# Optimization experiments

Measured on AMD Instinct MI355X. Metric: run time of the kernel, lower is better.

Reference implementation:

```python
import jax, jax.numpy as jnp
import numpy as np

N, E, F_IN, HID, NCLS, K, D = 50000, 800000, 128, 64, 16, 3, 2
EPS = 1e-15


def gmm_conv(x, src, dst, edge_attr, g, mu, sigma, root, bias):
    # x: [N, Fin]; g: [Fin, K*M]; mu, sigma: [K, D]; root: [Fin, M]; bias: [M]
    M = g.shape[1] // K
    h = x @ g                                        # [N, K*M]
    hj = h[src].reshape(-1, K, M)                    # edge gather [E, K, M]
    diff = edge_attr[:, None, :] - mu[None, :, :]    # [E, K, D]
    gauss = jnp.exp((-0.5 * diff * diff / (EPS + sigma[None] ** 2)).sum(-1))  # [E, K]
    msg = (hj * gauss[:, :, None]).sum(axis=1)       # [E, M]
    agg = jax.ops.segment_sum(msg, dst, num_segments=N)                  # scatter-add
    deg = jax.ops.segment_sum(jnp.ones(msg.shape[0], x.dtype), dst, num_segments=N)
    agg = agg / jnp.maximum(deg, 1.0)[:, None]       # mean aggregation
    return agg + x @ root + bias


def setup_inputs() -> dict:
    key = jax.random.key(0)
    ks = jax.random.split(key, 13)
    x = jax.random.normal(ks[0], (N, F_IN), jnp.float32)
    edge_index = jax.random.randint(ks[1], (2, E), 0, N, dtype=jnp.int64)
    edge_attr = jax.random.uniform(ks[2], (E, D), jnp.float32)
    s1 = 1.0 / np.sqrt(F_IN)
    s2 = 1.0 / np.sqrt(HID)
    return {
        "x": x,
        "edge_index": edge_index,
        "edge_attr": edge_attr,
        "g1": jax.random.normal(ks[3], (F_IN, K * HID), jnp.float32) * s1,
        "mu1": jax.random.normal(ks[4], (K, D), jnp.float32),
        "sigma1": jnp.ones((K, D), jnp.float32),
        "root1": jax.random.normal(ks[5], (F_IN, HID), jnp.float32) * s1,
        "b1": jnp.zeros((HID,), jnp.float32),
        "g2": jax.random.normal(ks[6], (HID, K * NCLS), jnp.float32) * s2,
        "mu2": jax.random.normal(ks[7], (K, D), jnp.float32),
        "sigma2": jnp.ones((K, D), jnp.float32),
        "root2": jax.random.normal(ks[8], (HID, NCLS), jnp.float32) * s2,
        "b2": jnp.zeros((NCLS,), jnp.float32),
    }


def reference(x, edge_index, edge_attr, g1, mu1, sigma1, root1, b1, g2, mu2, sigma2, root2, b2):
    # eval mode: dropout is identity
    src, dst = edge_index[0], edge_index[1]
    h = gmm_conv(x, src, dst, edge_attr, g1, mu1, sigma1, root1, b1)
    h = jax.nn.elu(h)
    out = gmm_conv(h, src, dst, edge_attr, g2, mu2, sigma2, root2, b2)
    return jax.nn.log_softmax(out, axis=1)
```

## Files before the change

### kernel.cpp

```cpp
#include <hip/hip_runtime.h>
#include <hip/hip_fp16.h>

#define EPS 1e-15f
#define BKT_SHIFT 7
#define BKT_SIZE 128
#define NBKT_MAX 512

typedef _Float16 v8h __attribute__((ext_vector_type(8)));
typedef float v4f __attribute__((ext_vector_type(4)));
typedef float v2f __attribute__((ext_vector_type(2)));

#if __has_builtin(__builtin_amdgcn_cvt_pk_f32_fp8) && __has_builtin(__builtin_amdgcn_cvt_pk_fp8_f32)
#define FP8_HW 1
#else
#define FP8_HW 0
#endif

__device__ __forceinline__ unsigned char f32_to_fp8(float v) {
#if FP8_HW
    int r = __builtin_amdgcn_cvt_pk_fp8_f32(v, v, 0, false);
    return (unsigned char)(r & 0xFF);
#else
    __half h = __float2half(v);
    unsigned short u; __builtin_memcpy(&u, &h, 2);
    int s = (u >> 15) << 7;
    int a = (u & 0x7FFF) + 0x40;
    if (a < (9 << 10)) return (unsigned char)s;
    int t = (a >> 7) - 64;
    if (t > 126) t = 126;
    return (unsigned char)(s | t);
#endif
}

__device__ __forceinline__ float2 fp8x2_to_f32(unsigned short w) {
#if FP8_HW
    v2f r = __builtin_amdgcn_cvt_pk_f32_fp8((int)w, false);
    return make_float2(r.x, r.y);
#else
    int b0 = w & 0xFF, b1 = w >> 8;
    unsigned short h0 = (unsigned short)((((b0 & 0x7F) + 64) << 7) | ((b0 & 0x80) << 8));
    unsigned short h1 = (unsigned short)((((b1 & 0x7F) + 64) << 7) | ((b1 & 0x80) << 8));
    __half x0, x1;
    __builtin_memcpy(&x0, &h0, 2);
    __builtin_memcpy(&x1, &h1, 2);
    return make_float2(__half2float(x0), __half2float(x1));
#endif
}

__device__ __forceinline__ int load_idx(const int* __restrict__ ei, int is64, int pos) {
    return is64 ? ei[(size_t)2 * pos] : ei[pos];
}

__device__ __forceinline__ int h2_as_int(__half2 h) {
    int w; __builtin_memcpy(&w, &h, 4); return w;
}
__device__ __forceinline__ __half2 int_as_h2(int w) {
    __half2 h; __builtin_memcpy(&h, &w, 4); return h;
}

__global__ void detect_kernel(const int* __restrict__ ei, int* __restrict__ flag,
                              int* __restrict__ bcnt, int nbkt) {
    __shared__ int any_odd;
    if (threadIdx.x == 0) any_odd = 0;
    __syncthreads();
    for (int u = threadIdx.x; u < nbkt; u += 256) bcnt[u] = 0;
    if (ei[2 * threadIdx.x + 1] != 0) atomicOr(&any_odd, 1);
    __syncthreads();
    if (threadIdx.x == 0) *flag = any_odd ? 0 : 1;
}

__global__ __launch_bounds__(256) void bhist_kernel(
    const int* __restrict__ ei, const int* __restrict__ flag,
    int* __restrict__ bcnt, int E, int nbkt) {
    __shared__ int cnt[NBKT_MAX];
    int t = threadIdx.x;
    for (int u = t; u < nbkt; u += 256) cnt[u] = 0;
    __syncthreads();
    int is64 = *flag;
    int e0 = blockIdx.x * 4096;
#pragma unroll
    for (int i = 0; i < 16; ++i) {
        int e = e0 + i * 256 + t;
        if (e < E) atomicAdd(&cnt[load_idx(ei, is64, E + e) >> BKT_SHIFT], 1);
    }
    __syncthreads();
    for (int u = t; u < nbkt; u += 256)
        if (cnt[u]) atomicAdd(&bcnt[u], cnt[u]);
}

__global__ void bscan_kernel(const int* __restrict__ bcnt, int* __restrict__ bbase,
                             int* __restrict__ bcursor, int* __restrict__ rowptrN,
                             int nbkt, int E) {
    __shared__ int s[512];
    int t = threadIdx.x;
    int v = (t < nbkt) ? bcnt[t] : 0;
    s[t] = v;
    __syncthreads();
    for (int o = 1; o < 512; o <<= 1) {
        int u = (t >= o) ? s[t - o] : 0;
        __syncthreads();
        s[t] += u;
        __syncthreads();
    }
    if (t < nbkt) { int ex = s[t] - v; bbase[t] = ex; bcursor[t] = ex; }
    if (t == 0) { bbase[nbkt] = E; *rowptrN = E; }
}

__global__ __launch_bounds__(1024) void pass1_kernel(
    const int* __restrict__ ei, const int* __restrict__ flag,
    const float2* __restrict__ ea, int* __restrict__ bcursor,
    int4* __restrict__ staging, int E, int nbkt) {
    __shared__ int lcnt[NBKT_MAX];
    __shared__ int lcur[NBKT_MAX];
    int t = threadIdx.x;
    if (t < nbkt) lcnt[t] = 0;
    __syncthreads();
    int is64 = *flag;
    int e0 = blockIdx.x * 8192;
    int eend = min(e0 + 8192, E);

    for (int e = e0 + t; e < eend; e += 1024)
        atomicAdd(&lcnt[load_idx(ei, is64, E + e) >> BKT_SHIFT], 1);
    __syncthreads();

    if (t < nbkt) {
        int c = lcnt[t];
        lcur[t] = c ? atomicAdd(&bcursor[t], c) : 0;
    }
    __syncthreads();

    for (int e = e0 + t; e < eend; e += 1024) {
        int src = load_idx(ei, is64, e);
        int dst = load_idx(ei, is64, E + e);
        float2 a = ea[e];
        int pos = atomicAdd(&lcur[dst >> BKT_SHIFT], 1);
        staging[pos] = make_int4(src, dst,
                                 __float_as_int(a.x), __float_as_int(a.y));
    }
}

__global__ __launch_bounds__(256) void pass2_kernel(
    const int4* __restrict__ staging, const int* __restrict__ bbase,
    const float* __restrict__ mu1, const float* __restrict__ sg1,
    const float* __restrict__ mu2, const float* __restrict__ sg2,
    int4* __restrict__ rec, int* __restrict__ rowptr, int N) {
    __shared__ int lcnt[BKT_SIZE];
    __shared__ int ssc[BKT_SIZE];
    __shared__ int lcur[BKT_SIZE];
    int b = blockIdx.x;
    int node0 = b << BKT_SHIFT;
    int t = threadIdx.x;
    int beg = bbase[b], end = bbase[b + 1];

    if (t < BKT_SIZE) lcnt[t] = 0;
    __syncthreads();
    for (int j = beg + t; j < end; j += 256)
        atomicAdd(&lcnt[staging[j].y & (BKT_SIZE - 1)], 1);
    __syncthreads();
    int v = (t < BKT_SIZE) ? lcnt[t] : 0;
    if (t < BKT_SIZE) ssc[t] = v;
    __syncthreads();
    for (int o = 1; o < BKT_SIZE; o <<= 1) {
        int u = (t < BKT_SIZE && t >= o) ? ssc[t - o] : 0;
        __syncthreads();
        if (t < BKT_SIZE) ssc[t] += u;
        __syncthreads();
    }
    if (t < BKT_SIZE) {
        int excl = beg + ssc[t] - v;
        lcur[t] = excl;
        if (node0 + t < N) rowptr[node0 + t] = excl;
    }
    __syncthreads();

    float m1x[3], m1y[3], i1x[3], i1y[3], m2x[3], m2y[3], i2x[3], i2y[3];
#pragma unroll
    for (int k = 0; k < 3; ++k) {
        m1x[k] = mu1[2 * k]; m1y[k] = mu1[2 * k + 1];
        float s0 = sg1[2 * k], s1 = sg1[2 * k + 1];
        i1x[k] = -0.5f / (EPS + s0 * s0); i1y[k] = -0.5f / (EPS + s1 * s1);
        m2x[k] = mu2[2 * k]; m2y[k] = mu2[2 * k + 1];
        s0 = sg2[2 * k]; s1 = sg2[2 * k + 1];
        i2x[k] = -0.5f / (EPS + s0 * s0); i2y[k] = -0.5f / (EPS + s1 * s1);
    }

    for (int j = beg + t; j < end; j += 256) {
        int4 p = staging[j];
        float ax = __int_as_float(p.z), ay = __int_as_float(p.w);
        float g1v[3], g2v[3];
#pragma unroll
        for (int k = 0; k < 3; ++k) {
            float d0 = ax - m1x[k], d1 = ay - m1y[k];
            g1v[k] = __expf(d0 * d0 * i1x[k] + d1 * d1 * i1y[k]);
            d0 = ax - m2x[k]; d1 = ay - m2y[k];
            g2v[k] = __expf(d0 * d0 * i2x[k] + d1 * d1 * i2y[k]);
        }
        int pos = atomicAdd(&lcur[p.y & (BKT_SIZE - 1)], 1);
        int4 r;
        r.x = p.x;
        r.y = h2_as_int(__floats2half2_rn(g1v[0], g1v[1]));
        r.z = h2_as_int(__floats2half2_rn(g1v[2], g2v[0]));
        r.w = h2_as_int(__floats2half2_rn(g2v[1], g2v[2]));
        rec[pos] = r;
    }
}

__global__ void bprep_kernel(const float* __restrict__ g1, const float* __restrict__ r1,
                             __half* __restrict__ Bprep) {
    int gid = blockIdx.x * 256 + threadIdx.x;
    if (gid >= 32768) return;
    int fi = gid >> 9;
    int lane = (gid >> 3) & 63;
    int i = gid & 7;
    int ks = fi & 3, cb = fi >> 2;
    int k = ks * 32 + (lane >> 4) * 8 + i;
    int c = cb * 16 + (lane & 15);
    float v = (c < 192) ? g1[k * 192 + c] : r1[k * 64 + (c - 192)];
    Bprep[gid] = __float2half(v);
}

__global__ __launch_bounds__(256) void gemm1_mfma(
    const float* __restrict__ A, const __half* __restrict__ Bprep,
    unsigned char* __restrict__ hw1k, __half* __restrict__ hw1r, int M) {
    __shared__ char a_lds[64 * 256];
    int row0 = blockIdx.x * 64;
    int tid = threadIdx.x;
    int wid = tid >> 6, lane = tid & 63;

    const float4* xf4 = reinterpret_cast<const float4*>(A);
#pragma unroll
    for (int j = 0; j < 8; ++j) {
        int g = j * 256 + tid;
        int r = g >> 5, c = g & 31;
        int gr = row0 + r;
        float4 f = (gr < M) ? xf4[(size_t)gr * 32 + c]
                            : make_float4(0.f, 0.f, 0.f, 0.f);
        int2 v;
        v.x = h2_as_int(__floats2half2_rn(f.x, f.y));
        v.y = h2_as_int(__floats2half2_rn(f.z, f.w));
        int byte = r * 256 + c * 8;
        byte ^= (r & 7) << 4;
        *reinterpret_cast<int2*>(&a_lds[byte]) = v;
    }

    v8h bf[2][4];
#pragma unroll
    for (int cf = 0; cf < 2; ++cf)
#pragma unroll
        for (int ks = 0; ks < 4; ++ks) {
            int cb = blockIdx.y * 8 + wid * 2 + cf;
            int fi = cb * 4 + ks;
            bf[cf][ks] = *reinterpret_cast<const v8h*>(Bprep + (size_t)fi * 512 + lane * 8);
        }

    __syncthreads();

    v4f acc[4][2] = {};
#pragma unroll
    for (int ks = 0; ks < 4; ++ks) {
        v8h af[4];
#pragma unroll
        for (int rf = 0; rf < 4; ++rf) {
            int r = rf * 16 + (lane & 15);
            int byte = r * 256 + ks * 64 + (lane >> 4) * 16;
            byte ^= (r & 7) << 4;
            af[rf] = *reinterpret_cast<const v8h*>(&a_lds[byte]);
        }
#pragma unroll
        for (int rf = 0; rf < 4; ++rf)
#pragma unroll
            for (int cf = 0; cf < 2; ++cf)
                acc[rf][cf] = __builtin_amdgcn_mfma_f32_16x16x32_f16(
                    af[rf], bf[cf][ks], acc[rf][cf], 0, 0, 0);
    }

#pragma unroll
    for (int rf = 0; rf < 4; ++rf)
#pragma unroll
        for (int cf = 0; cf < 2; ++cf) {
            int gc = blockIdx.y * 128 + wid * 32 + cf * 16 + (lane & 15);
#pragma unroll
            for (int i = 0; i < 4; ++i) {
                int gr = row0 + rf * 16 + (lane >> 4) * 4 + i;
                if (gr < M) {
                    float val = acc[rf][cf][i];
                    if (gc < 192)
                        hw1k[(size_t)gr * 192 + gc] = f32_to_fp8(val);
                    else
                        hw1r[(size_t)gr * 64 + (gc - 192)] = __float2half(val);
                }
            }
        }
}

__global__ __launch_bounds__(256) void agg1_fused(
    const int4* __restrict__ rec, const int* __restrict__ rowptr,
    const unsigned char* __restrict__ hw1k, const __half* __restrict__ hw1r,
    const float* __restrict__ b1, const float* __restrict__ g2,
    const float* __restrict__ r2, __half* __restrict__ hw2h, int N) {
    __shared__ float Wlds[64][64];
    __shared__ float h2s[8][64];
    int t = threadIdx.x;

    for (int i = t; i < 4096; i += 256) {
        int k = i >> 6, c = i & 63;
        Wlds[k][c] = (c < 48) ? g2[k * 48 + c] : r2[k * 16 + (c - 48)];
    }

    int node = (blockIdx.x * 256 + t) >> 5;
    int nl = (t >> 5) & 7;
    int l = t & 31;
    bool active = node < N;

    float ax0 = 0.f, ay0 = 0.f, ax1 = 0.f, ay1 = 0.f;
    int beg = 0, end = 0;
    if (active) { beg = rowptr[node]; end = rowptr[node + 1]; }
    int j = beg;
    for (; j + 3 < end; j += 4) {
        int4 r0 = rec[j], r1 = rec[j + 1], r2v = rec[j + 2], r3 = rec[j + 3];
        const unsigned short* p0 = reinterpret_cast<const unsigned short*>(
            hw1k + (size_t)r0.x * 192);
        const unsigned short* p1 = reinterpret_cast<const unsigned short*>(
            hw1k + (size_t)r1.x * 192);
        const unsigned short* p2 = reinterpret_cast<const unsigned short*>(
            hw1k + (size_t)r2v.x * 192);
        const unsigned short* p3 = reinterpret_cast<const unsigned short*>(
            hw1k + (size_t)r3.x * 192);
        unsigned short w00 = p0[l], w01 = p0[32 + l], w02 = p0[64 + l];
        unsigned short w10 = p1[l], w11 = p1[32 + l], w12 = p1[64 + l];
        unsigned short w20 = p2[l], w21 = p2[32 + l], w22 = p2[64 + l];
        unsigned short w30 = p3[l], w31 = p3[32 + l], w32 = p3[64 + l];
        __half2 ha0 = int_as_h2(r0.y), hb0 = int_as_h2(r0.z);
        __half2 ha1 = int_as_h2(r1.y), hb1 = int_as_h2(r1.z);
        __half2 ha2 = int_as_h2(r2v.y), hb2 = int_as_h2(r2v.z);
        __half2 ha3 = int_as_h2(r3.y), hb3 = int_as_h2(r3.z);
        {
            float g0 = __low2float(ha0), g1 = __high2float(ha0), gg2 = __low2float(hb0);
            float2 a = fp8x2_to_f32(w00), b = fp8x2_to_f32(w01), c = fp8x2_to_f32(w02);
            ax0 += g0 * a.x + g1 * b.x + gg2 * c.x;
            ay0 += g0 * a.y + g1 * b.y + gg2 * c.y;
        }
        {
            float g0 = __low2float(ha1), g1 = __high2float(ha1), gg2 = __low2float(hb1);
            float2 a = fp8x2_to_f32(w10), b = fp8x2_to_f32(w11), c = fp8x2_to_f32(w12);
            ax1 += g0 * a.x + g1 * b.x + gg2 * c.x;
            ay1 += g0 * a.y + g1 * b.y + gg2 * c.y;
        }
        {
            float g0 = __low2float(ha2), g1 = __high2float(ha2), gg2 = __low2float(hb2);
            float2 a = fp8x2_to_f32(w20), b = fp8x2_to_f32(w21), c = fp8x2_to_f32(w22);
            ax0 += g0 * a.x + g1 * b.x + gg2 * c.x;
            ay0 += g0 * a.y + g1 * b.y + gg2 * c.y;
        }
        {
            float g0 = __low2float(ha3), g1 = __high2float(ha3), gg2 = __low2float(hb3);
            float2 a = fp8x2_to_f32(w30), b = fp8x2_to_f32(w31), c = fp8x2_to_f32(w32);
            ax1 += g0 * a.x + g1 * b.x + gg2 * c.x;
            ay1 += g0 * a.y + g1 * b.y + gg2 * c.y;
        }
    }
    for (; j < end; ++j) {
        int4 r0 = rec[j];
        __half2 ha0 = int_as_h2(r0.y), hb0 = int_as_h2(r0.z);
        float g0 = __low2float(ha0), g1 = __high2float(ha0), gg2 = __low2float(hb0);
        const unsigned short* p0 = reinterpret_cast<const unsigned short*>(
            hw1k + (size_t)r0.x * 192);
        float2 a = fp8x2_to_f32(p0[l]);
        float2 b = fp8x2_to_f32(p0[32 + l]);
        float2 c = fp8x2_to_f32(p0[64 + l]);
        ax0 += g0 * a.x + g1 * b.x + gg2 * c.x;
        ay0 += g0 * a.y + g1 * b.y + gg2 * c.y;
    }
    if (active) {
        float d = fmaxf((float)(end - beg), 1.0f);
        float2 root = __half22float2(
            reinterpret_cast<const __half2*>(hw1r + (size_t)node * 64)[l]);
        float2 bb = reinterpret_cast<const float2*>(b1)[l];
        float v0 = (ax0 + ax1) / d + root.x + bb.x;
        float v1 = (ay0 + ay1) / d + root.y + bb.y;
        h2s[nl][2 * l]     = v0 > 0.f ? v0 : expm1f(v0);
        h2s[nl][2 * l + 1] = v1 > 0.f ? v1 : expm1f(v1);
    }
    __syncthreads();

    if (active) {
        float acc0 = 0.f, acc1 = 0.f;
#pragma unroll 8
        for (int k = 0; k < 64; ++k) {
            float hv = h2s[nl][k];
            float2 w = *reinterpret_cast<const float2*>(&Wlds[k][2 * l]);
            acc0 += hv * w.x;
            acc1 += hv * w.y;
        }
        reinterpret_cast<__half2*>(hw2h)[(size_t)node * 32 + l] =
            __floats2half2_rn(acc0, acc1);
    }
}

__global__ __launch_bounds__(256) void agg2_kernel(
    const int4* __restrict__ rec, const int* __restrict__ rowptr,
    const __half* __restrict__ hw2h, const float* __restrict__ b2,
    float* __restrict__ out, int N) {
    int node = (blockIdx.x * 256 + threadIdx.x) >> 3;
    int l = threadIdx.x & 7;
    if (node >= N) return;
    int beg = rowptr[node], end = rowptr[node + 1];
    float ax = 0.f, ay = 0.f;
    for (int j = beg; j < end; ++j) {
        int4 r = rec[j];
        __half2 hb = int_as_h2(r.z), hc = int_as_h2(r.w);
        float g0 = __high2float(hb), g1 = __low2float(hc), g2 = __high2float(hc);
        const __half2* p = reinterpret_cast<const __half2*>(hw2h + (size_t)r.x * 64);
        float2 f0 = __half22float2(p[l]);
        float2 f1 = __half22float2(p[8 + l]);
        float2 f2 = __half22float2(p[16 + l]);
        ax += g0 * f0.x + g1 * f1.x + g2 * f2.x;
        ay += g0 * f0.y + g1 * f1.y + g2 * f2.y;
    }
    float d = fmaxf((float)(end - beg), 1.0f);
    float2 root = __half22float2(
        reinterpret_cast<const __half2*>(hw2h + (size_t)node * 64 + 48)[l]);
    float2 bb = reinterpret_cast<const float2*>(b2)[l];
    float v0 = ax / d + root.x + bb.x;
    float v1 = ay / d + root.y + bb.y;

    float mx = fmaxf(v0, v1);
#pragma unroll
    for (int off = 4; off >= 1; off >>= 1) mx = fmaxf(mx, __shfl_xor(mx, off, 8));
    float s = __expf(v0 - mx) + __expf(v1 - mx);
#pragma unroll
    for (int off = 4; off >= 1; off >>= 1) s += __shfl_xor(s, off, 8);
    float ls = __logf(s);
    float2 o = make_float2(v0 - mx - ls, v1 - mx - ls);
    reinterpret_cast<float2*>(out + (size_t)node * 16)[l] = o;
}

extern "C" void kernel_launch(void* const* d_in, const int* in_sizes, int n_in,
                              void* d_out, int out_size, void* d_ws, size_t ws_size,
                              hipStream_t stream) {
    const float* x   = (const float*)d_in[0];
    const int*   ei  = (const int*)d_in[1];
    const float* ea  = (const float*)d_in[2];
    const float* g1  = (const float*)d_in[3];
    const float* mu1 = (const float*)d_in[4];
    const float* sg1 = (const float*)d_in[5];
    const float* r1  = (const float*)d_in[6];
    const float* b1  = (const float*)d_in[7];
    const float* g2  = (const float*)d_in[8];
    const float* mu2 = (const float*)d_in[9];
    const float* sg2 = (const float*)d_in[10];
    const float* r2  = (const float*)d_in[11];
    const float* b2  = (const float*)d_in[12];

    const int N = in_sizes[0] / 128;
    const int E = in_sizes[2] / 2;
    const int nbkt = (N + BKT_SIZE - 1) >> BKT_SHIFT;

    unsigned char* hw1k = (unsigned char*)d_ws;
    __half* hw1r = (__half*)(hw1k + (size_t)N * 192);
    __half* hw2h = (__half*)(hw1r + (size_t)N * 64);
    int4*   rec  = (int4*)(hw2h + (size_t)N * 64);
    int4*   staging = rec + E;
    __half* Bprep = (__half*)(staging + E);
    int*    rowptr  = (int*)(Bprep + 32768);
    int*    bcnt    = rowptr + N + 1;
    int*    bbase   = bcnt + nbkt;
    int*    bcursor = bbase + nbkt + 1;
    int*    flag    = bcursor + nbkt;

    detect_kernel<<<1, 256, 0, stream>>>(ei, flag, bcnt, nbkt);
    bhist_kernel<<<(E + 4095) / 4096, 256, 0, stream>>>(ei, flag, bcnt, E, nbkt);
    bscan_kernel<<<1, 512, 0, stream>>>(bcnt, bbase, bcursor, rowptr + N, nbkt, E);

    pass1_kernel<<<(E + 8191) / 8192, 1024, 0, stream>>>(
        ei, flag, (const float2*)ea, bcursor, staging, E, nbkt);
    pass2_kernel<<<nbkt, 256, 0, stream>>>(
        staging, bbase, mu1, sg1, mu2, sg2, rec, rowptr, N);

    bprep_kernel<<<128, 256, 0, stream>>>(g1, r1, Bprep);
    gemm1_mfma<<<dim3((N + 63) / 64, 2), 256, 0, stream>>>(x, Bprep, hw1k, hw1r, N);

    agg1_fused<<<((size_t)N * 32 + 255) / 256, 256, 0, stream>>>(
        rec, rowptr, hw1k, hw1r, b1, g2, r2, hw2h, N);

    agg2_kernel<<<((size_t)N * 8 + 255) / 256, 256, 0, stream>>>(
        rec, rowptr, hw2h, b2, (float*)d_out, N);
}
```

Before: 133.1 us.

## Balance agg1 edge work across block via LDS atomics with packed dst-local index

Instead of one 32-lane group per destination node walking its own edge list, each block now takes the contiguous edge range of its 8 nodes and spreads the edges round-robin over the 8 groups, accumulating into shared memory with float atomics. The local destination index is packed into the top byte of the source id in the edge record, and agg2 masks it off. This evens out work when node degrees differ, at the cost of LDS atomic contention, the loss of the 4-way unrolled loads, and a source id limited to 24 bits. Atomic ordering also makes the summation order nondeterministic.

```diff
diff --git a/kernel.cpp b/kernel.cpp
--- a/kernel.cpp
+++ b/kernel.cpp
@@ -195,9 +195,10 @@
             d0 = ax - m2x[k]; d1 = ay - m2y[k];
             g2v[k] = __expf(d0 * d0 * i2x[k] + d1 * d1 * i2y[k]);
         }
-        int pos = atomicAdd(&lcur[p.y & (BKT_SIZE - 1)], 1);
+        int dl = p.y & (BKT_SIZE - 1);
+        int pos = atomicAdd(&lcur[dl], 1);
         int4 r;
-        r.x = p.x;
+        r.x = p.x | (dl << 24);
         r.y = h2_as_int(__floats2half2_rn(g1v[0], g1v[1]));
         r.z = h2_as_int(__floats2half2_rn(g1v[2], g2v[0]));
         r.w = h2_as_int(__floats2half2_rn(g2v[1], g2v[2]));
@@ -299,101 +300,69 @@
     const float* __restrict__ b1, const float* __restrict__ g2,
     const float* __restrict__ r2, __half* __restrict__ hw2h, int N) {
     __shared__ float Wlds[64][64];
-    __shared__ float h2s[8][64];
+    __shared__ float h2a[8][64];
+    __shared__ int rp[9];
     int t = threadIdx.x;
+    int node0 = blockIdx.x * 8;
 
     for (int i = t; i < 4096; i += 256) {
         int k = i >> 6, c = i & 63;
         Wlds[k][c] = (c < 48) ? g2[k * 48 + c] : r2[k * 16 + (c - 48)];
     }
-
-    int node = (blockIdx.x * 256 + t) >> 5;
-    int nl = (t >> 5) & 7;
-    int l = t & 31;
-    bool active = node < N;
-
-    float ax0 = 0.f, ay0 = 0.f, ax1 = 0.f, ay1 = 0.f;
-    int beg = 0, end = 0;
-    if (active) { beg = rowptr[node]; end = rowptr[node + 1]; }
-    int j = beg;
-    for (; j + 3 < end; j += 4) {
-        int4 r0 = rec[j], r1 = rec[j + 1], r2v = rec[j + 2], r3 = rec[j + 3];
-        const unsigned short* p0 = reinterpret_cast<const unsigned short*>(
-            hw1k + (size_t)r0.x * 192);
-        const unsigned short* p1 = reinterpret_cast<const unsigned short*>(
-            hw1k + (size_t)r1.x * 192);
-        const unsigned short* p2 = reinterpret_cast<const unsigned short*>(
-            hw1k + (size_t)r2v.x * 192);
-        const unsigned short* p3 = reinterpret_cast<const unsigned short*>(
-            hw1k + (size_t)r3.x * 192);
-        unsigned short w00 = p0[l], w01 = p0[32 + l], w02 = p0[64 + l];
-        unsigned short w10 = p1[l], w11 = p1[32 + l], w12 = p1[64 + l];
-        unsigned short w20 = p2[l], w21 = p2[32 + l], w22 = p2[64 + l];
-        unsigned short w30 = p3[l], w31 = p3[32 + l], w32 = p3[64 + l];
-        __half2 ha0 = int_as_h2(r0.y), hb0 = int_as_h2(r0.z);
-        __half2 ha1 = int_as_h2(r1.y), hb1 = int_as_h2(r1.z);
-        __half2 ha2 = int_as_h2(r2v.y), hb2 = int_as_h2(r2v.z);
-        __half2 ha3 = int_as_h2(r3.y), hb3 = int_as_h2(r3.z);
-        {
-            float g0 = __low2float(ha0), g1 = __high2float(ha0), gg2 = __low2float(hb0);
-            float2 a = fp8x2_to_f32(w00), b = fp8x2_to_f32(w01), c = fp8x2_to_f32(w02);
-            ax0 += g0 * a.x + g1 * b.x + gg2 * c.x;
-            ay0 += g0 * a.y + g1 * b.y + gg2 * c.y;
-        }
-        {
-            float g0 = __low2float(ha1), g1 = __high2float(ha1), gg2 = __low2float(hb1);
-            float2 a = fp8x2_to_f32(w10), b = fp8x2_to_f32(w11), c = fp8x2_to_f32(w12);
-            ax1 += g0 * a.x + g1 * b.x + gg2 * c.x;
-            ay1 += g0 * a.y + g1 * b.y + gg2 * c.y;
-        }
-        {
-            float g0 = __low2float(ha2), g1 = __high2float(ha2), gg2 = __low2float(hb2);
-            float2 a = fp8x2_to_f32(w20), b = fp8x2_to_f32(w21), c = fp8x2_to_f32(w22);
-            ax0 += g0 * a.x + g1 * b.x + gg2 * c.x;
-            ay0 += g0 * a.y + g1 * b.y + gg2 * c.y;
-        }
-        {
-            float g0 = __low2float(ha3), g1 = __high2float(ha3), gg2 = __low2float(hb3);
-            float2 a = fp8x2_to_f32(w30), b = fp8x2_to_f32(w31), c = fp8x2_to_f32(w32);
-            ax1 += g0 * a.x + g1 * b.x + gg2 * c.x;
-            ay1 += g0 * a.y + g1 * b.y + gg2 * c.y;
-        }
-    }
-    for (; j < end; ++j) {
-        int4 r0 = rec[j];
-        __half2 ha0 = int_as_h2(r0.y), hb0 = int_as_h2(r0.z);
-        float g0 = __low2float(ha0), g1 = __high2float(ha0), gg2 = __low2float(hb0);
-        const unsigned short* p0 = reinterpret_cast<const unsigned short*>(
-            hw1k + (size_t)r0.x * 192);
-        float2 a = fp8x2_to_f32(p0[l]);
-        float2 b = fp8x2_to_f32(p0[32 + l]);
-        float2 c = fp8x2_to_f32(p0[64 + l]);
-        ax0 += g0 * a.x + g1 * b.x + gg2 * c.x;
-        ay0 += g0 * a.y + g1 * b.y + gg2 * c.y;
-    }
-    if (active) {
-        float d = fmaxf((float)(end - beg), 1.0f);
-        float2 root = __half22float2(
-            reinterpret_cast<const __half2*>(hw1r + (size_t)node * 64)[l]);
-        float2 bb = reinterpret_cast<const float2*>(b1)[l];
-        float v0 = (ax0 + ax1) / d + root.x + bb.x;
-        float v1 = (ay0 + ay1) / d + root.y + bb.y;
-        h2s[nl][2 * l]     = v0 > 0.f ? v0 : expm1f(v0);
-        h2s[nl][2 * l + 1] = v1 > 0.f ? v1 : expm1f(v1);
-    }
-    __syncthreads();
-
-    if (active) {
-        float acc0 = 0.f, acc1 = 0.f;
+    reinterpret_cast<float2*>(&h2a[0][0])[t] = make_float2(0.f, 0.f);
+    int nn = min(8, N - node0);
+    if (t <= nn) rp[t] = rowptr[node0 + t];
+    __syncthreads();
+
+    int beg = rp[0], end = rp[nn];
+    int g = t >> 5, l = t & 31;
+
+    for (int j = beg + g; j < end; j += 8) {
+        int4 r = rec[j];
+        int src = r.x & 0xFFFFFF;
+        int nl = (r.x >> 24) & 7;
+        __half2 ha = int_as_h2(r.y), hb = int_as_h2(r.z);
+        float g0 = __low2float(ha), g1 = __high2float(ha), gg2 = __low2float(hb);
+        const unsigned short* p = reinterpret_cast<const unsigned short*>(
+            hw1k + (size_t)src * 192);
+        float2 a = fp8x2_to_f32(p[l]);
+        float2 b = fp8x2_to_f32(p[32 + l]);
+        float2 c = fp8x2_to_f32(p[64 + l]);
+        atomicAdd(&h2a[nl][2 * l],     g0 * a.x + g1 * b.x + gg2 * c.x);
+        atomicAdd(&h2a[nl][2 * l + 1], g0 * a.y + g1 * b.y + gg2 * c.y);
+    }
+    __syncthreads();
+
+    {
+        int nl = t >> 5;
+        if (nl < nn) {
+            int gn = node0 + nl;
+            float d = fmaxf((float)(rp[nl + 1] - rp[nl]), 1.f);
+            float2 root = __half22float2(
+                reinterpret_cast<const __half2*>(hw1r + (size_t)gn * 64)[l]);
+            float2 bb = reinterpret_cast<const float2*>(b1)[l];
+            float v0 = h2a[nl][2 * l] / d + root.x + bb.x;
+            float v1 = h2a[nl][2 * l + 1] / d + root.y + bb.y;
+            h2a[nl][2 * l]     = v0 > 0.f ? v0 : expm1f(v0);
+            h2a[nl][2 * l + 1] = v1 > 0.f ? v1 : expm1f(v1);
+        }
+    }
+    __syncthreads();
+
+    {
+        int nl = t >> 5;
+        if (nl < nn) {
+            float acc0 = 0.f, acc1 = 0.f;
 #pragma unroll 8
-        for (int k = 0; k < 64; ++k) {
-            float hv = h2s[nl][k];
-            float2 w = *reinterpret_cast<const float2*>(&Wlds[k][2 * l]);
-            acc0 += hv * w.x;
-            acc1 += hv * w.y;
-        }
-        reinterpret_cast<__half2*>(hw2h)[(size_t)node * 32 + l] =
-            __floats2half2_rn(acc0, acc1);
+            for (int k = 0; k < 64; ++k) {
+                float hv = h2a[nl][k];
+                float2 w = *reinterpret_cast<const float2*>(&Wlds[k][2 * l]);
+                acc0 += hv * w.x;
+                acc1 += hv * w.y;
+            }
+            reinterpret_cast<__half2*>(hw2h)[(size_t)(node0 + nl) * 32 + l] =
+                __floats2half2_rn(acc0, acc1);
+        }
     }
 }
 
@@ -408,9 +377,10 @@
     float ax = 0.f, ay = 0.f;
     for (int j = beg; j < end; ++j) {
         int4 r = rec[j];
+        int src = r.x & 0xFFFFFF;
         __half2 hb = int_as_h2(r.z), hc = int_as_h2(r.w);
         float g0 = __high2float(hb), g1 = __low2float(hc), g2 = __high2float(hc);
-        const __half2* p = reinterpret_cast<const __half2*>(hw2h + (size_t)r.x * 64);
+        const __half2* p = reinterpret_cast<const __half2*>(hw2h + (size_t)src * 64);
         float2 f0 = __half22float2(p[l]);
         float2 f1 = __half22float2(p[8 + l]);
         float2 f2 = __half22float2(p[16 + l]);
@@ -480,7 +450,7 @@
     bprep_kernel<<<128, 256, 0, stream>>>(g1, r1, Bprep);
     gemm1_mfma<<<dim3((N + 63) / 64, 2), 256, 0, stream>>>(x, Bprep, hw1k, hw1r, N);
 
-    agg1_fused<<<((size_t)N * 32 + 255) / 256, 256, 0, stream>>>(
+    agg1_fused<<<(N + 7) / 8, 256, 0, stream>>>(
         rec, rowptr, hw1k, hw1r, b1, g2, r2, hw2h, N);
 
     agg2_kernel<<<((size_t)N * 8 + 255) / 256, 256, 0, stream>>>(
```

Measured after the change: 376.2 us. 2.83x slower.
